# Kernel optimization log

Measured on AMD Instinct MI355X. Metric: run time of the kernel, lower is better.

## Reference

```python
import jax, jax.numpy as jnp
import numpy as np

N_NODES = 50000
N_EDGES = 800000
DIM = 128
N_LAYERS = 5
BN_EPS = 1e-5


def setup_inputs() -> dict:
    key = jax.random.key(0)
    ks = jax.random.split(key, 8)
    x = jax.random.normal(ks[0], (N_NODES, DIM), dtype=jnp.float32)
    edge_index = jax.random.randint(ks[1], (2, N_EDGES), 0, N_NODES, dtype=jnp.int64)
    batch = jnp.sort(jax.random.randint(ks[2], (N_NODES,), 0, 64, dtype=jnp.int64))
    scale = 1.0 / np.sqrt(DIM)
    W1 = jax.random.normal(ks[3], (N_LAYERS, DIM, DIM), dtype=jnp.float32) * scale
    b1 = jnp.zeros((N_LAYERS, DIM), dtype=jnp.float32)
    W2 = jax.random.normal(ks[4], (N_LAYERS, DIM, DIM), dtype=jnp.float32) * scale
    b2 = jnp.zeros((N_LAYERS, DIM), dtype=jnp.float32)
    gamma = jnp.ones((N_LAYERS, DIM), dtype=jnp.float32)
    beta = jnp.zeros((N_LAYERS, DIM), dtype=jnp.float32)
    return {"x": x, "edge_index": edge_index, "batch": batch,
            "W1": W1, "b1": b1, "W2": W2, "b2": b2,
            "gamma": gamma, "beta": beta}


def _gin_layer(x, src, dst, w1, bb1, w2, bb2, g, b):
    # GINConv (eps=0): h_i = MLP(x_i + sum_{j->i} x_j)
    agg = jax.ops.segment_sum(x[src], dst, num_segments=N_NODES)  # [N, D]
    h = x + agg
    h = jnp.maximum(h @ w1 + bb1, 0.0) @ w2 + bb2  # 2-layer MLP
    h = jnp.maximum(h, 0.0)                        # outer ReLU
    # BatchNorm1d (training-mode batch stats, biased variance)
    mu = jnp.mean(h, axis=0)
    var = jnp.mean(jnp.square(h - mu), axis=0)
    return (h - mu) * jax.lax.rsqrt(var + BN_EPS) * g + b


def reference(x, edge_index, batch, W1, b1, W2, b2, gamma, beta):
    src, dst = edge_index[0], edge_index[1]
    xs = []
    h = x
    for i in range(N_LAYERS):
        h = _gin_layer(h, src, dst, W1[i], b1[i], W2[i], b2[i], gamma[i], beta[i])
        xs.append(h)
    return h, jnp.stack(xs)
```

## Files before the change

### kernel.cpp

```cpp
#include <hip/hip_runtime.h>

#define N_NODES 50000
#define DIM 128
#define N_LAYERS 5
#define BN_EPS 1e-5f

typedef __attribute__((ext_vector_type(8))) short short8;
typedef __attribute__((ext_vector_type(4))) float f32x4;

__device__ __forceinline__ float bf2f(unsigned int u16) {
    union { unsigned int i; float f; } c; c.i = u16 << 16; return c.f;
}
__device__ __forceinline__ unsigned short f2bf(float f) {
    union { float f; unsigned int i; } c; c.f = f;
    unsigned int v = c.i + 0x7FFFu + ((c.i >> 16) & 1u);
    return (unsigned short)(v >> 16);
}


__global__ void hist_kernel(const int* __restrict__ dst, int n_edges, int* __restrict__ counts) {
    int e = blockIdx.x * 256 + threadIdx.x;
    if (e < n_edges) atomicAdd(&counts[dst[e]], 1);
}

__global__ void scan_local(const int* __restrict__ counts, int n,
                           int* __restrict__ offsets, int* __restrict__ blocksums) {
    __shared__ int temp[256];
    int t = threadIdx.x;
    int i = blockIdx.x * 256 + t;
    int v = (i < n) ? counts[i] : 0;
    temp[t] = v;
    __syncthreads();
    for (int off = 1; off < 256; off <<= 1) {
        int add = (t >= off) ? temp[t - off] : 0;
        __syncthreads();
        temp[t] += add;
        __syncthreads();
    }
    if (i < n) offsets[i] = temp[t] - v;
    if (t == 255) blocksums[blockIdx.x] = temp[255];
}

__global__ void scan_block(int* __restrict__ blocksums, int nb) {
    __shared__ int temp[256];
    int t = threadIdx.x;
    int v = (t < nb) ? blocksums[t] : 0;
    temp[t] = v;
    __syncthreads();
    for (int off = 1; off < 256; off <<= 1) {
        int add = (t >= off) ? temp[t - off] : 0;
        __syncthreads();
        temp[t] += add;
        __syncthreads();
    }
    if (t < nb) blocksums[t] = temp[t] - v;
}

__global__ void scan_add(int* __restrict__ offsets, int* __restrict__ cursor,
                         const int* __restrict__ blocksums, int n, int n_edges) {
    int i = blockIdx.x * 256 + threadIdx.x;
    if (i < n) {
        int val = offsets[i] + blocksums[blockIdx.x];
        offsets[i] = val;
        cursor[i] = val;
    }
    if (i == 0) offsets[n] = n_edges;
}

__global__ void scatter_kernel(const int* __restrict__ src, const int* __restrict__ dst,
                               int n_edges, int* __restrict__ cursor, int* __restrict__ csr_src) {
    int e = blockIdx.x * 256 + threadIdx.x;
    if (e < n_edges) {
        int p = atomicAdd(&cursor[dst[e]], 1);
        csr_src[p] = src[e];
    }
}


__global__ void wpack_prep(const float* __restrict__ W1, const float* __restrict__ W2,
                           unsigned short* __restrict__ wp) {
    int idx = blockIdx.x * 256 + threadIdx.x;
    if (idx >= N_LAYERS * 2 * 16384) return;
    int j    = idx & 7;
    int lane = (idx >> 3) & 63;
    int nt   = (idx >> 9) & 7;
    int ks   = (idx >> 12) & 3;
    int mat  = (idx >> 14) & 1;
    int lay  = idx >> 15;
    int l15 = lane & 15, l4 = lane >> 4;
    int col = nt * 16 + l15;
    int kp = ks * 32 + l4 * 8 + j;
    int k = mat ? ((kp & 7) * 16 + (kp >> 3)) : kp;
    const float* W = mat ? W2 : W1;
    float w = W[((size_t)lay * 128 + k) * 128 + col];
    unsigned short hi = f2bf(w);
    unsigned short lo = f2bf(w - bf2f(hi));
    size_t base = (size_t)(lay * 2 + mat) * 32768;
    size_t inner = (size_t)((ks * 8 + nt) * 64 + lane) * 8 + j;
    wp[base + inner] = hi;
    wp[base + 16384 + inner] = lo;
}


__global__ void agg_kernel(const float* __restrict__ x, const int* __restrict__ csr_src,
                           const int* __restrict__ offsets,
                           unsigned int* __restrict__ h_hi_u, unsigned int* __restrict__ h_lo_u) {
    int wave = threadIdx.x >> 6;
    int lane = threadIdx.x & 63;
    int node = blockIdx.x * 4 + wave;
    if (node >= N_NODES) return;
    int beg = offsets[node], end = offsets[node + 1];
    const float2* x2 = (const float2*)x;
    float2 acc = x2[(size_t)node * 64 + lane];

    for (int e = beg; e < end; e += 8) {
        int s[8];
#pragma unroll
        for (int i = 0; i < 8; ++i) s[i] = csr_src[min(e + i, end - 1)];
        float2 v[8];
#pragma unroll
        for (int i = 0; i < 8; ++i) v[i] = x2[(size_t)s[i] * 64 + lane];
#pragma unroll
        for (int i = 0; i < 8; ++i) {
            float w = (e + i < end) ? 1.0f : 0.0f;
            acc.x = fmaf(v[i].x, w, acc.x);
            acc.y = fmaf(v[i].y, w, acc.y);
        }
    }

    unsigned short hx = f2bf(acc.x), hy = f2bf(acc.y);
    unsigned short lx = f2bf(acc.x - bf2f(hx)), ly = f2bf(acc.y - bf2f(hy));
    h_hi_u[node * 64 + lane] = (unsigned int)hx | ((unsigned int)hy << 16);
    h_lo_u[node * 64 + lane] = (unsigned int)lx | ((unsigned int)ly << 16);
}

__global__ __launch_bounds__(128) void mlp_mfma(
        const unsigned short* __restrict__ h_hi, const unsigned short* __restrict__ h_lo,
        const short8* __restrict__ wp1, const float* __restrict__ b1,
        const short8* __restrict__ wp2, const float* __restrict__ b2,
        float* __restrict__ h_raw,
        float* __restrict__ part_s, float* __restrict__ part_q) {
    __shared__ unsigned short mid_hi[2][2][16][128];
    __shared__ unsigned short mid_lo[2][2][16][128];
    __shared__ float red_s[2][128], red_q[2][128];
    int t = threadIdx.x, wave = t >> 6, l = t & 63;
    int l15 = l & 15, l4 = l >> 4;
    int row_base = blockIdx.x * 64 + wave * 32;

    int r0 = row_base + l15, r1 = r0 + 16;
    int cr0 = min(r0, N_NODES - 1), cr1 = min(r1, N_NODES - 1);
    const short8* ah0p = (const short8*)(h_hi + (size_t)cr0 * 128);
    const short8* ah1p = (const short8*)(h_hi + (size_t)cr1 * 128);
    const short8* al0p = (const short8*)(h_lo + (size_t)cr0 * 128);
    const short8* al1p = (const short8*)(h_lo + (size_t)cr1 * 128);

    const short8* wp1l = wp1 + 2048;
    const short8* wp2l = wp2 + 2048;

    f32x4 acc[2][8];
#pragma unroll
    for (int m = 0; m < 2; ++m)
#pragma unroll
        for (int nt = 0; nt < 8; ++nt) acc[m][nt] = (f32x4)0.0f;

#pragma unroll
    for (int ks = 0; ks < 4; ++ks) {
        short8 ah0 = ah0p[ks * 4 + l4];
        short8 ah1 = ah1p[ks * 4 + l4];
        short8 al0 = al0p[ks * 4 + l4];
        short8 al1 = al1p[ks * 4 + l4];
#pragma unroll
        for (int nt = 0; nt < 8; ++nt) {
            short8 whi = wp1[(ks * 8 + nt) * 64 + l];
            short8 wlo = wp1l[(ks * 8 + nt) * 64 + l];
            acc[0][nt] = __builtin_amdgcn_mfma_f32_16x16x32_bf16(ah0, whi, acc[0][nt], 0, 0, 0);
            acc[0][nt] = __builtin_amdgcn_mfma_f32_16x16x32_bf16(al0, whi, acc[0][nt], 0, 0, 0);
            acc[0][nt] = __builtin_amdgcn_mfma_f32_16x16x32_bf16(ah0, wlo, acc[0][nt], 0, 0, 0);
            acc[1][nt] = __builtin_amdgcn_mfma_f32_16x16x32_bf16(ah1, whi, acc[1][nt], 0, 0, 0);
            acc[1][nt] = __builtin_amdgcn_mfma_f32_16x16x32_bf16(al1, whi, acc[1][nt], 0, 0, 0);
            acc[1][nt] = __builtin_amdgcn_mfma_f32_16x16x32_bf16(ah1, wlo, acc[1][nt], 0, 0, 0);
        }
    }

    float b1v[8];
#pragma unroll
    for (int nt = 0; nt < 8; ++nt) b1v[nt] = b1[nt * 16 + l15];

#pragma unroll
    for (int m = 0; m < 2; ++m) {
#pragma unroll
        for (int rr = 0; rr < 4; ++rr) {
            int row = l4 * 4 + rr;
            short8 ph, pl;
#pragma unroll
            for (int nt = 0; nt < 8; ++nt) {
                float v = fmaxf(acc[m][nt][rr] + b1v[nt], 0.0f);
                unsigned short hv = f2bf(v);
                ph[nt] = (short)hv;
                pl[nt] = (short)f2bf(v - bf2f(hv));
            }
            int off = (l15 * 16) ^ ((row & 7) << 4);
            *(short8*)((char*)&mid_hi[wave][m][row][0] + off) = ph;
            *(short8*)((char*)&mid_lo[wave][m][row][0] + off) = pl;
        }
    }
    __syncthreads();

    f32x4 acc2[2][8];
#pragma unroll
    for (int m = 0; m < 2; ++m)
#pragma unroll
        for (int nt = 0; nt < 8; ++nt) acc2[m][nt] = (f32x4)0.0f;

#pragma unroll
    for (int ks = 0; ks < 4; ++ks) {
        int off = (ks * 64 + l4 * 16) ^ ((l15 & 7) << 4);
        short8 ah0 = *(const short8*)((char*)&mid_hi[wave][0][l15][0] + off);
        short8 ah1 = *(const short8*)((char*)&mid_hi[wave][1][l15][0] + off);
        short8 al0 = *(const short8*)((char*)&mid_lo[wave][0][l15][0] + off);
        short8 al1 = *(const short8*)((char*)&mid_lo[wave][1][l15][0] + off);
#pragma unroll
        for (int nt = 0; nt < 8; ++nt) {
            short8 whi = wp2[(ks * 8 + nt) * 64 + l];
            short8 wlo = wp2l[(ks * 8 + nt) * 64 + l];
            acc2[0][nt] = __builtin_amdgcn_mfma_f32_16x16x32_bf16(ah0, whi, acc2[0][nt], 0, 0, 0);
            acc2[0][nt] = __builtin_amdgcn_mfma_f32_16x16x32_bf16(al0, whi, acc2[0][nt], 0, 0, 0);
            acc2[0][nt] = __builtin_amdgcn_mfma_f32_16x16x32_bf16(ah0, wlo, acc2[0][nt], 0, 0, 0);
            acc2[1][nt] = __builtin_amdgcn_mfma_f32_16x16x32_bf16(ah1, whi, acc2[1][nt], 0, 0, 0);
            acc2[1][nt] = __builtin_amdgcn_mfma_f32_16x16x32_bf16(al1, whi, acc2[1][nt], 0, 0, 0);
            acc2[1][nt] = __builtin_amdgcn_mfma_f32_16x16x32_bf16(ah1, wlo, acc2[1][nt], 0, 0, 0);
        }
    }

    float b2v[8];
#pragma unroll
    for (int nt = 0; nt < 8; ++nt) b2v[nt] = b2[nt * 16 + l15];

    float s[8], q[8];
#pragma unroll
    for (int nt = 0; nt < 8; ++nt) { s[nt] = 0.0f; q[nt] = 0.0f; }

#pragma unroll
    for (int m = 0; m < 2; ++m) {
#pragma unroll
        for (int rr = 0; rr < 4; ++rr) {
            int rg = row_base + m * 16 + l4 * 4 + rr;
            bool ok = rg < N_NODES;
#pragma unroll
            for (int nt = 0; nt < 8; ++nt) {
                float v = fmaxf(acc2[m][nt][rr] + b2v[nt], 0.0f);
                if (ok) {
                    h_raw[(size_t)rg * 128 + nt * 16 + l15] = v;
                    s[nt] += v;
                    q[nt] += v * v;
                }
            }
        }
    }
#pragma unroll
    for (int nt = 0; nt < 8; ++nt) {
        s[nt] += __shfl_xor(s[nt], 16); s[nt] += __shfl_xor(s[nt], 32);
        q[nt] += __shfl_xor(q[nt], 16); q[nt] += __shfl_xor(q[nt], 32);
    }
    if (l4 == 0) {
#pragma unroll
        for (int nt = 0; nt < 8; ++nt) {
            red_s[wave][nt * 16 + l15] = s[nt];
            red_q[wave][nt * 16 + l15] = q[nt];
        }
    }
    __syncthreads();
    if (t < 128) {
        part_s[blockIdx.x * 128 + t] = red_s[0][t] + red_s[1][t];
        part_q[blockIdx.x * 128 + t] = red_q[0][t] + red_q[1][t];
    }
}

__global__ __launch_bounds__(256) void bn_reduce(
        const float* __restrict__ part_s, const float* __restrict__ part_q,
        float* __restrict__ bn_sum, float* __restrict__ bn_sq, int nparts) {
    __shared__ float red[256];
    int c = blockIdx.x & 127;
    const float* src = (blockIdx.x >> 7) ? part_q : part_s;
    float* dst = (blockIdx.x >> 7) ? bn_sq : bn_sum;
    float a = 0.0f;
    for (int p = threadIdx.x; p < nparts; p += 256) a += src[p * 128 + c];
    red[threadIdx.x] = a;
    __syncthreads();
    for (int s = 128; s > 0; s >>= 1) {
        if (threadIdx.x < s) red[threadIdx.x] += red[threadIdx.x + s];
        __syncthreads();
    }
    if (threadIdx.x == 0) dst[c] = red[0];
}

__global__ void bn_apply(float* __restrict__ h,
                         const float* __restrict__ bn_sum, const float* __restrict__ bn_sq,
                         const float* __restrict__ gamma, const float* __restrict__ beta,
                         float4* __restrict__ dup) {
    int i4 = blockIdx.x * 256 + threadIdx.x;
    if (i4 >= N_NODES * DIM / 4) return;
    float4 v = ((const float4*)h)[i4];
    int c0 = (i4 & 31) * 4;
    const float invN = 1.0f / (float)N_NODES;
    float* vp = (float*)&v;
#pragma unroll
    for (int j = 0; j < 4; ++j) {
        int c = c0 + j;
        float mean = bn_sum[c] * invN;
        float var = fmaxf(bn_sq[c] * invN - mean * mean, 0.0f);
        float inv = rsqrtf(var + BN_EPS);
        vp[j] = (vp[j] - mean) * inv * gamma[c] + beta[c];
    }
    ((float4*)h)[i4] = v;
    if (dup) dup[i4] = v;
}


extern "C" void kernel_launch(void* const* d_in, const int* in_sizes, int n_in,
                              void* d_out, int out_size, void* d_ws, size_t ws_size,
                              hipStream_t stream) {
    const float* x     = (const float*)d_in[0];
    const int*   eidx  = (const int*)d_in[1];
    const float* W1    = (const float*)d_in[3];
    const float* b1    = (const float*)d_in[4];
    const float* W2    = (const float*)d_in[5];
    const float* b2    = (const float*)d_in[6];
    const float* gamma = (const float*)d_in[7];
    const float* beta  = (const float*)d_in[8];

    int n_edges = in_sizes[1] / 2;
    const int* src = eidx;
    const int* dst = eidx + n_edges;

    const int NBLK = (N_NODES + 63) / 64;

    int* counts    = (int*)d_ws;
    int* offsets   = counts + N_NODES;
    int* cursor    = offsets + N_NODES + 1;
    int* blocksums = cursor + N_NODES;
    int* csr_src   = blocksums + 256;
    float* part_s  = (float*)(csr_src + n_edges);
    float* part_q  = part_s + NBLK * 128;
    float* bn_sum  = part_q + NBLK * 128;
    float* bn_sq   = bn_sum + DIM;
    size_t wp_off = (((size_t)(bn_sq + DIM) - (size_t)d_ws) + 15) & ~(size_t)15;
    unsigned short* wp = (unsigned short*)((char*)d_ws + wp_off);

    float* out = (float*)d_out;
    unsigned int* h_hi_u = (unsigned int*)d_out;
    unsigned int* h_lo_u = h_hi_u + (size_t)N_NODES * 64;
    const unsigned short* h_hi = (const unsigned short*)h_hi_u;
    const unsigned short* h_lo = (const unsigned short*)h_lo_u;

    hipMemsetAsync(counts, 0, N_NODES * sizeof(int), stream);
    hist_kernel<<<(n_edges + 255) / 256, 256, 0, stream>>>(dst, n_edges, counts);
    int nb = (N_NODES + 255) / 256;
    scan_local<<<nb, 256, 0, stream>>>(counts, N_NODES, offsets, blocksums);
    scan_block<<<1, 256, 0, stream>>>(blocksums, nb);
    scan_add<<<nb, 256, 0, stream>>>(offsets, cursor, blocksums, N_NODES, n_edges);
    scatter_kernel<<<(n_edges + 255) / 256, 256, 0, stream>>>(src, dst, n_edges, cursor, csr_src);

    wpack_prep<<<(N_LAYERS * 2 * 16384 + 255) / 256, 256, 0, stream>>>(W1, W2, wp);

    const float* layer_in = x;
    for (int i = 0; i < N_LAYERS; ++i) {
        float* layer_out = out + (size_t)(1 + i) * N_NODES * DIM;
        agg_kernel<<<(N_NODES + 3) / 4, 256, 0, stream>>>(layer_in, csr_src, offsets,
                                                          h_hi_u, h_lo_u);
        mlp_mfma<<<NBLK, 128, 0, stream>>>(
            h_hi, h_lo,
            (const short8*)(wp + (size_t)(i * 2) * 32768), b1 + (size_t)i * DIM,
            (const short8*)(wp + (size_t)(i * 2 + 1) * 32768), b2 + (size_t)i * DIM,
            layer_out, part_s, part_q);
        bn_reduce<<<256, 256, 0, stream>>>(part_s, part_q, bn_sum, bn_sq, NBLK);
        bn_apply<<<(N_NODES * DIM / 4 + 255) / 256, 256, 0, stream>>>(
            layer_out, bn_sum, bn_sq, gamma + (size_t)i * DIM, beta + (size_t)i * DIM,
            (i == N_LAYERS - 1) ? (float4*)out : (float4*)nullptr);
        layer_in = layer_out;
    }
}
```

Measured before the change: 606.3 us.

## Fold BatchNorm into aggregation and gather from an fp16 feature table

The MLP output is stored as pre-BN fp16 values, and the per-node BatchNorm affine is applied inside the next layer's aggregation using linearity: A*sum + B*(degree+1). The separate bn_apply pass per layer is removed, except for a final pass on the last layer. Gathers read 16-byte fp16 rows, with four edge groups per wave reduced by shuffles. This halves gather bandwidth and removes a full read/write of the activations per layer. In exchange, inputs and intermediate activations are rounded to fp16, which lowers precision.

```diff
diff --git a/kernel.cpp b/kernel.cpp
--- a/kernel.cpp
+++ b/kernel.cpp
@@ -1,4 +1,5 @@
 #include <hip/hip_runtime.h>
+#include <hip/hip_fp16.h>
 
 #define N_NODES 50000
 #define DIM 128
@@ -15,6 +16,14 @@
     union { float f; unsigned int i; } c; c.f = f;
     unsigned int v = c.i + 0x7FFFu + ((c.i >> 16) & 1u);
     return (unsigned short)(v >> 16);
+}
+__device__ __forceinline__ unsigned short f2h(float f) {
+    __half h = __float2half(f);
+    return *reinterpret_cast<unsigned short*>(&h);
+}
+__device__ __forceinline__ float h2f(unsigned short u) {
+    __half h = *reinterpret_cast<__half*>(&u);
+    return __half2float(h);
 }
 
 
@@ -101,44 +110,121 @@
     wp[base + 16384 + inner] = lo;
 }
 
-
-__global__ void agg_kernel(const float* __restrict__ x, const int* __restrict__ csr_src,
-                           const int* __restrict__ offsets,
-                           unsigned int* __restrict__ h_hi_u, unsigned int* __restrict__ h_lo_u) {
+__global__ void convert_x_f16(const float4* __restrict__ x, uint2* __restrict__ xh, int n4) {
+    int i = blockIdx.x * 256 + threadIdx.x;
+    if (i >= n4) return;
+    float4 v = x[i];
+    uint2 o;
+    o.x = (unsigned int)f2h(v.x) | ((unsigned int)f2h(v.y) << 16);
+    o.y = (unsigned int)f2h(v.z) | ((unsigned int)f2h(v.w) << 16);
+    xh[i] = o;
+}
+
+__global__ void agg_f16(const uint4* __restrict__ tbl4, const int* __restrict__ csr_src,
+                        const int* __restrict__ offsets,
+                        const float* __restrict__ bn_sum, const float* __restrict__ bn_sq,
+                        const float* __restrict__ gamma, const float* __restrict__ beta,
+                        float* __restrict__ xs_out,
+                        unsigned int* __restrict__ h_hi_u, unsigned int* __restrict__ h_lo_u) {
     int wave = threadIdx.x >> 6;
-    int lane = threadIdx.x & 63;
+    int l = threadIdx.x & 63;
     int node = blockIdx.x * 4 + wave;
     if (node >= N_NODES) return;
+    int g = l >> 4;
+    int d = l & 15;
     int beg = offsets[node], end = offsets[node + 1];
-    const float2* x2 = (const float2*)x;
-    float2 acc = x2[(size_t)node * 64 + lane];
-
-    for (int e = beg; e < end; e += 8) {
+
+    float self[8];
+    float a[8];
+#pragma unroll
+    for (int j = 0; j < 8; ++j) { a[j] = 0.0f; self[j] = 0.0f; }
+    if (g == 0) {
+        uint4 u = tbl4[(size_t)node * 16 + d];
+        self[0] = h2f(u.x & 0xFFFFu); self[1] = h2f(u.x >> 16);
+        self[2] = h2f(u.y & 0xFFFFu); self[3] = h2f(u.y >> 16);
+        self[4] = h2f(u.z & 0xFFFFu); self[5] = h2f(u.z >> 16);
+        self[6] = h2f(u.w & 0xFFFFu); self[7] = h2f(u.w >> 16);
+#pragma unroll
+        for (int j = 0; j < 8; ++j) a[j] = self[j];
+    }
+
+    for (int e = beg; e < end; e += 32) {
         int s[8];
 #pragma unroll
-        for (int i = 0; i < 8; ++i) s[i] = csr_src[min(e + i, end - 1)];
-        float2 v[8];
-#pragma unroll
-        for (int i = 0; i < 8; ++i) v[i] = x2[(size_t)s[i] * 64 + lane];
+        for (int i = 0; i < 8; ++i) s[i] = csr_src[min(e + 4 * i + g, end - 1)];
+        uint4 v[8];
+#pragma unroll
+        for (int i = 0; i < 8; ++i) v[i] = tbl4[(size_t)s[i] * 16 + d];
 #pragma unroll
         for (int i = 0; i < 8; ++i) {
-            float w = (e + i < end) ? 1.0f : 0.0f;
-            acc.x = fmaf(v[i].x, w, acc.x);
-            acc.y = fmaf(v[i].y, w, acc.y);
-        }
-    }
-
-    unsigned short hx = f2bf(acc.x), hy = f2bf(acc.y);
-    unsigned short lx = f2bf(acc.x - bf2f(hx)), ly = f2bf(acc.y - bf2f(hy));
-    h_hi_u[node * 64 + lane] = (unsigned int)hx | ((unsigned int)hy << 16);
-    h_lo_u[node * 64 + lane] = (unsigned int)lx | ((unsigned int)ly << 16);
+            float w = (e + 4 * i + g < end) ? 1.0f : 0.0f;
+            a[0] = fmaf(h2f(v[i].x & 0xFFFFu), w, a[0]);
+            a[1] = fmaf(h2f(v[i].x >> 16),     w, a[1]);
+            a[2] = fmaf(h2f(v[i].y & 0xFFFFu), w, a[2]);
+            a[3] = fmaf(h2f(v[i].y >> 16),     w, a[3]);
+            a[4] = fmaf(h2f(v[i].z & 0xFFFFu), w, a[4]);
+            a[5] = fmaf(h2f(v[i].z >> 16),     w, a[5]);
+            a[6] = fmaf(h2f(v[i].w & 0xFFFFu), w, a[6]);
+            a[7] = fmaf(h2f(v[i].w >> 16),     w, a[7]);
+        }
+    }
+
+#pragma unroll
+    for (int j = 0; j < 8; ++j) {
+        a[j] += __shfl_xor(a[j], 16);
+        a[j] += __shfl_xor(a[j], 32);
+    }
+
+    if (bn_sum) {
+        const float invN = 1.0f / (float)N_NODES;
+        float cnt = (float)(end - beg + 1);
+#pragma unroll
+        for (int j = 0; j < 8; ++j) {
+            int c = d * 8 + j;
+            float mean = bn_sum[c] * invN;
+            float var = fmaxf(bn_sq[c] * invN - mean * mean, 0.0f);
+            float inv = rsqrtf(var + BN_EPS);
+            float A = gamma[c] * inv;
+            float B = beta[c] - mean * A;
+            a[j] = A * a[j] + B * cnt;
+            self[j] = A * self[j] + B;
+        }
+    }
+
+    unsigned short h[8];
+#pragma unroll
+    for (int j = 0; j < 8; ++j) h[j] = f2bf(a[j]);
+    if (g == 0) {
+        uint4 hv;
+        hv.x = (unsigned int)h[0] | ((unsigned int)h[1] << 16);
+        hv.y = (unsigned int)h[2] | ((unsigned int)h[3] << 16);
+        hv.z = (unsigned int)h[4] | ((unsigned int)h[5] << 16);
+        hv.w = (unsigned int)h[6] | ((unsigned int)h[7] << 16);
+        ((uint4*)h_hi_u)[(size_t)node * 16 + d] = hv;
+        if (xs_out) {
+            float4 o0 = make_float4(self[0], self[1], self[2], self[3]);
+            float4 o1 = make_float4(self[4], self[5], self[6], self[7]);
+            ((float4*)xs_out)[(size_t)node * 32 + d * 2]     = o0;
+            ((float4*)xs_out)[(size_t)node * 32 + d * 2 + 1] = o1;
+        }
+    } else if (g == 1) {
+        unsigned short lo[8];
+#pragma unroll
+        for (int j = 0; j < 8; ++j) lo[j] = f2bf(a[j] - bf2f(h[j]));
+        uint4 lv;
+        lv.x = (unsigned int)lo[0] | ((unsigned int)lo[1] << 16);
+        lv.y = (unsigned int)lo[2] | ((unsigned int)lo[3] << 16);
+        lv.z = (unsigned int)lo[4] | ((unsigned int)lo[5] << 16);
+        lv.w = (unsigned int)lo[6] | ((unsigned int)lo[7] << 16);
+        ((uint4*)h_lo_u)[(size_t)node * 16 + d] = lv;
+    }
 }
 
 __global__ __launch_bounds__(128) void mlp_mfma(
         const unsigned short* __restrict__ h_hi, const unsigned short* __restrict__ h_lo,
         const short8* __restrict__ wp1, const float* __restrict__ b1,
         const short8* __restrict__ wp2, const float* __restrict__ b2,
-        float* __restrict__ h_raw,
+        unsigned short* __restrict__ raw_h,
         float* __restrict__ part_s, float* __restrict__ part_q) {
     __shared__ unsigned short mid_hi[2][2][16][128];
     __shared__ unsigned short mid_lo[2][2][16][128];
@@ -250,7 +336,7 @@
             for (int nt = 0; nt < 8; ++nt) {
                 float v = fmaxf(acc2[m][nt][rr] + b2v[nt], 0.0f);
                 if (ok) {
-                    h_raw[(size_t)rg * 128 + nt * 16 + l15] = v;
+                    raw_h[(size_t)rg * 128 + nt * 16 + l15] = f2h(v);
                     s[nt] += v;
                     q[nt] += v * v;
                 }
@@ -294,26 +380,29 @@
     if (threadIdx.x == 0) dst[c] = red[0];
 }
 
-__global__ void bn_apply(float* __restrict__ h,
-                         const float* __restrict__ bn_sum, const float* __restrict__ bn_sq,
-                         const float* __restrict__ gamma, const float* __restrict__ beta,
-                         float4* __restrict__ dup) {
+__global__ void bn_apply_last(const uint2* __restrict__ hraw,
+                              float4* __restrict__ xs, float4* __restrict__ fin,
+                              const float* __restrict__ bn_sum, const float* __restrict__ bn_sq,
+                              const float* __restrict__ gamma, const float* __restrict__ beta) {
     int i4 = blockIdx.x * 256 + threadIdx.x;
     if (i4 >= N_NODES * DIM / 4) return;
-    float4 v = ((const float4*)h)[i4];
+    uint2 u = hraw[i4];
+    float vv[4] = { h2f(u.x & 0xFFFFu), h2f(u.x >> 16),
+                    h2f(u.y & 0xFFFFu), h2f(u.y >> 16) };
     int c0 = (i4 & 31) * 4;
     const float invN = 1.0f / (float)N_NODES;
-    float* vp = (float*)&v;
+    float4 o;
+    float* op = (float*)&o;
 #pragma unroll
     for (int j = 0; j < 4; ++j) {
         int c = c0 + j;
         float mean = bn_sum[c] * invN;
         float var = fmaxf(bn_sq[c] * invN - mean * mean, 0.0f);
         float inv = rsqrtf(var + BN_EPS);
-        vp[j] = (vp[j] - mean) * inv * gamma[c] + beta[c];
-    }
-    ((float4*)h)[i4] = v;
-    if (dup) dup[i4] = v;
+        op[j] = (vv[j] - mean) * inv * gamma[c] + beta[c];
+    }
+    xs[i4] = o;
+    fin[i4] = o;
 }
 
 
@@ -346,6 +435,8 @@
     float* bn_sq   = bn_sum + DIM;
     size_t wp_off = (((size_t)(bn_sq + DIM) - (size_t)d_ws) + 15) & ~(size_t)15;
     unsigned short* wp = (unsigned short*)((char*)d_ws + wp_off);
+    size_t tb_off = (wp_off + (size_t)N_LAYERS * 2 * 32768 * 2 + 15) & ~(size_t)15;
+    unsigned short* tbl = (unsigned short*)((char*)d_ws + tb_off);
 
     float* out = (float*)d_out;
     unsigned int* h_hi_u = (unsigned int*)d_out;
@@ -362,21 +453,28 @@
     scatter_kernel<<<(n_edges + 255) / 256, 256, 0, stream>>>(src, dst, n_edges, cursor, csr_src);
 
     wpack_prep<<<(N_LAYERS * 2 * 16384 + 255) / 256, 256, 0, stream>>>(W1, W2, wp);
-
-    const float* layer_in = x;
+    convert_x_f16<<<(N_NODES * DIM / 4 + 255) / 256, 256, 0, stream>>>(
+        (const float4*)x, (uint2*)tbl, N_NODES * DIM / 4);
+
+    const int AGG_BLKS = (N_NODES + 3) / 4;
     for (int i = 0; i < N_LAYERS; ++i) {
-        float* layer_out = out + (size_t)(1 + i) * N_NODES * DIM;
-        agg_kernel<<<(N_NODES + 3) / 4, 256, 0, stream>>>(layer_in, csr_src, offsets,
-                                                          h_hi_u, h_lo_u);
+        agg_f16<<<AGG_BLKS, 256, 0, stream>>>(
+            (const uint4*)tbl, csr_src, offsets,
+            (i > 0) ? bn_sum : (const float*)nullptr, bn_sq,
+            (i > 0) ? gamma + (size_t)(i - 1) * DIM : (const float*)nullptr,
+            (i > 0) ? beta + (size_t)(i - 1) * DIM : (const float*)nullptr,
+            (i > 0) ? out + (size_t)i * N_NODES * DIM : (float*)nullptr,
+            h_hi_u, h_lo_u);
         mlp_mfma<<<NBLK, 128, 0, stream>>>(
             h_hi, h_lo,
             (const short8*)(wp + (size_t)(i * 2) * 32768), b1 + (size_t)i * DIM,
             (const short8*)(wp + (size_t)(i * 2 + 1) * 32768), b2 + (size_t)i * DIM,
-            layer_out, part_s, part_q);
+            tbl, part_s, part_q);
         bn_reduce<<<256, 256, 0, stream>>>(part_s, part_q, bn_sum, bn_sq, NBLK);
-        bn_apply<<<(N_NODES * DIM / 4 + 255) / 256, 256, 0, stream>>>(
-            layer_out, bn_sum, bn_sq, gamma + (size_t)i * DIM, beta + (size_t)i * DIM,
-            (i == N_LAYERS - 1) ? (float4*)out : (float4*)nullptr);
-        layer_in = layer_out;
-    }
-}
+    }
+    bn_apply_last<<<(N_NODES * DIM / 4 + 255) / 256, 256, 0, stream>>>(
+        (const uint2*)tbl,
+        (float4*)(out + (size_t)N_LAYERS * N_NODES * DIM), (float4*)out,
+        bn_sum, bn_sq, gamma + (size_t)(N_LAYERS - 1) * DIM,
+        beta + (size_t)(N_LAYERS - 1) * DIM);
+}
```

Result: faster. 533.1 us (-12.1%).
